# Kernel optimization log

Hardware: AMD Instinct MI355X
Metric: run time of the kernel (lower is better)

## Reference

```python
import jax, jax.numpy as jnp
import numpy as np

NH, NP, HD = 8, 4, 32  # num_heads, num_points, head_dim (C=256)


def setup_inputs() -> dict:
    key = jax.random.key(0)
    k = jax.random.split(key, 8)
    B, Nq, H, W, C = 4, 8192, 128, 128, 256
    query = jax.random.normal(k[0], (B, Nq, C), jnp.float32)
    reference_points = jax.random.uniform(k[1], (B, Nq, 2), jnp.float32)
    value = jax.random.normal(k[2], (B, H * W, C), jnp.float32)
    s = 1.0 / np.sqrt(C).astype(np.float32)
    W_off = jax.random.normal(k[3], (C, NH * NP * 2), jnp.float32) * s
    b_off = jax.random.normal(k[4], (NH * NP * 2,), jnp.float32) * 0.5
    W_attn = jax.random.normal(k[5], (C, NH * NP), jnp.float32) * s
    b_attn = jnp.zeros((NH * NP,), jnp.float32)
    W_val = jax.random.normal(k[6], (C, C), jnp.float32) * s
    b_val = jnp.zeros((C,), jnp.float32)
    W_out = jax.random.normal(k[7], (C, C), jnp.float32) * s
    b_out = jnp.zeros((C,), jnp.float32)
    return dict(query=query, reference_points=reference_points, value=value,
                W_off=W_off, b_off=b_off, W_attn=W_attn, b_attn=b_attn,
                W_val=W_val, b_val=b_val, W_out=W_out, b_out=b_out, Hs=H, Ws=W)


def reference(query, reference_points, value, W_off, b_off, W_attn, b_attn,
              W_val, b_val, W_out, b_out, Hs, Ws):
    B, Nq, C = query.shape
    # sampling offsets and attention weights from queries
    off = (query @ W_off + b_off).reshape(B, Nq, NH, NP, 2)
    attn = jax.nn.softmax((query @ W_attn + b_attn).reshape(B, Nq, NH, NP), axis=-1)
    off = jnp.stack([off[..., 0] / Ws * 0.1, off[..., 1] / Hs * 0.1], axis=-1)
    loc = jnp.clip(reference_points[:, :, None, None, :] + off, 0.0, 1.0)  # [B,Nq,NH,NP,2] (x,y)
    # project value and arrange per head: [B, NH, H*W, HD]
    v = (value @ W_val + b_val).reshape(B, Hs, Ws, NH, HD)
    v = v.transpose(0, 3, 1, 2, 4).reshape(B, NH, Hs * Ws, HD)
    # grid_sample bilinear, align_corners=False, padding_mode='border':
    # pixel coord = loc*size - 0.5, clamped to [0, size-1]
    gx = jnp.clip(loc[..., 0] * Ws - 0.5, 0.0, Ws - 1.0)
    gy = jnp.clip(loc[..., 1] * Hs - 0.5, 0.0, Hs - 1.0)
    x0 = jnp.floor(gx); y0 = jnp.floor(gy)
    fx = gx - x0; fy = gy - y0
    x0i = x0.astype(jnp.int32); y0i = y0.astype(jnp.int32)
    x1i = jnp.minimum(x0i + 1, Ws - 1); y1i = jnp.minimum(y0i + 1, Hs - 1)

    def flat(xi, yi):  # [B,Nq,NH,NP] -> [B,NH,Nq*NP]
        return (yi * Ws + xi).transpose(0, 2, 1, 3).reshape(B, NH, Nq * NP)

    def gather(idx):  # -> [B,NH,Nq*NP,HD]
        return jnp.take_along_axis(v, idx[..., None], axis=2)

    def wts(w):  # [B,Nq,NH,NP] -> [B,NH,Nq*NP,1]
        return w.transpose(0, 2, 1, 3).reshape(B, NH, Nq * NP, 1)

    samp = (wts((1 - fx) * (1 - fy)) * gather(flat(x0i, y0i))
            + wts(fx * (1 - fy)) * gather(flat(x1i, y0i))
            + wts((1 - fx) * fy) * gather(flat(x0i, y1i))
            + wts(fx * fy) * gather(flat(x1i, y1i)))
    samp = samp.reshape(B, NH, Nq, NP, HD)
    aw = attn.transpose(0, 2, 1, 3)[..., None]  # [B,NH,Nq,NP,1]
    out = (samp * aw).sum(axis=3)               # [B,NH,Nq,HD]
    out = out.transpose(0, 2, 1, 3).reshape(B, Nq, C)
    return out @ W_out + b_out
```

## Files before the change

### kernel.cpp

```cpp
#include <hip/hip_runtime.h>
#include <cstddef>

#define B_   4
#define NQ_  8192
#define C_   256
#define H_   128
#define W_   128
#define HW_  (H_ * W_)
#define NH_  8
#define NP_  4
#define HD_  32

typedef __attribute__((ext_vector_type(8))) short s16x8;
typedef __attribute__((ext_vector_type(4))) float f32x4;

__device__ __forceinline__ short f2bf(float x) {
    unsigned u = __float_as_uint(x);
    unsigned r = (u + 0x7FFFu + ((u >> 16) & 1u)) >> 16;
    return (short)r;
}
__device__ __forceinline__ void gload_lds16(const void* g, void* l) {
    __builtin_amdgcn_global_load_lds(
        (const __attribute__((address_space(1))) void*)g,
        (__attribute__((address_space(3))) void*)l, 16, 0, 0);
}

__global__ void prep_kernel(const float* __restrict__ Wv, const float* __restrict__ Wo,
                            const float* __restrict__ Woff, const float* __restrict__ Wattn,
                            const float* __restrict__ boff, const float* __restrict__ battn,
                            short* __restrict__ BtVal, short* __restrict__ BtOut,
                            short* __restrict__ BtOA, float* __restrict__ biasOA)
{
    const int b = blockIdx.x, t = threadIdx.x;
    if (b < 256) {
        const int n = b;
        BtVal[(size_t)n * 256 + t] = f2bf(Wv[(size_t)t * 256 + n]);
    } else if (b < 512) {
        const int n = b - 256;
        BtOut[(size_t)n * 256 + t] = f2bf(Wo[(size_t)t * 256 + n]);
    } else {
        const int n = b - 512;
        float v = (n < 64) ? Woff[(size_t)t * 64 + n]
                           : (n < 96 ? Wattn[(size_t)t * 32 + (n - 64)] : 0.f);
        BtOA[(size_t)n * 256 + t] = f2bf(v);
        if (t == 0) biasOA[n] = (n < 64) ? boff[n] : (n < 96 ? battn[n - 64] : 0.f);
    }
}

template<int AMODE, int OMODE>
__global__ __launch_bounds__(256)
void gemm_mfma(const void* __restrict__ Ap, const short* __restrict__ Bt,
               const float* __restrict__ bias, void* __restrict__ Cp, int ldc)
{
    __shared__ short As[128 * 32];
    __shared__ short Bs[128 * 32];
    const int tid = threadIdx.x;
    const int l = tid & 63;
    const int w = tid >> 6;
    const int wm = w >> 1, wn = w & 1;
    const int m0 = blockIdx.x * 128;
    const int n0 = blockIdx.y * 128;

    f32x4 acc[4][4];
#pragma unroll
    for (int i = 0; i < 4; ++i)
#pragma unroll
        for (int j = 0; j < 4; ++j) acc[i][j] = (f32x4)0.f;

    const int frag_r = l & 15;
    const int kslot  = (l >> 4) * 8;

    for (int k0 = 0; k0 < 256; k0 += 32) {
        __syncthreads();
#pragma unroll
        for (int r = 0; r < 2; ++r) {
            const int i = r * 256 + tid;
            const int row = i >> 2, cb = (i & 3) * 8;
            gload_lds16(&Bt[(size_t)(n0 + row) * 256 + k0 + cb],
                        (char*)Bs + r * 4096 + w * 1024);
        }
        if (AMODE == 0) {
            const short* A16 = (const short*)Ap;
#pragma unroll
            for (int r = 0; r < 2; ++r) {
                const int i = r * 256 + tid;
                const int row = i >> 2, cb = (i & 3) * 8;
                gload_lds16(&A16[(size_t)(m0 + row) * 256 + k0 + cb],
                            (char*)As + r * 4096 + w * 1024);
            }
        } else {
            const float* Af = (const float*)Ap;
            const int row = tid >> 1, half = tid & 1;
            const float* src = &Af[(size_t)(m0 + row) * 256 + k0 + half * 16];
            float4 f0 = ((const float4*)src)[0];
            float4 f1 = ((const float4*)src)[1];
            float4 f2 = ((const float4*)src)[2];
            float4 f3 = ((const float4*)src)[3];
            union { short s[8]; s16x8 v; } p0, p1;
            p0.s[0]=f2bf(f0.x); p0.s[1]=f2bf(f0.y); p0.s[2]=f2bf(f0.z); p0.s[3]=f2bf(f0.w);
            p0.s[4]=f2bf(f1.x); p0.s[5]=f2bf(f1.y); p0.s[6]=f2bf(f1.z); p0.s[7]=f2bf(f1.w);
            p1.s[0]=f2bf(f2.x); p1.s[1]=f2bf(f2.y); p1.s[2]=f2bf(f2.z); p1.s[3]=f2bf(f2.w);
            p1.s[4]=f2bf(f3.x); p1.s[5]=f2bf(f3.y); p1.s[6]=f2bf(f3.z); p1.s[7]=f2bf(f3.w);
            *(s16x8*)&As[row * 32 + half * 16]     = p0.v;
            *(s16x8*)&As[row * 32 + half * 16 + 8] = p1.v;
        }
        __syncthreads();
        s16x8 a[4], b[4];
#pragma unroll
        for (int mf = 0; mf < 4; ++mf)
            a[mf] = *(const s16x8*)&As[(wm * 64 + mf * 16 + frag_r) * 32 + kslot];
#pragma unroll
        for (int nf = 0; nf < 4; ++nf)
            b[nf] = *(const s16x8*)&Bs[(wn * 64 + nf * 16 + frag_r) * 32 + kslot];
#pragma unroll
        for (int mf = 0; mf < 4; ++mf)
#pragma unroll
            for (int nf = 0; nf < 4; ++nf)
                acc[mf][nf] = __builtin_amdgcn_mfma_f32_16x16x32_bf16(
                    a[mf], b[nf], acc[mf][nf], 0, 0, 0);
    }

    const int col_local = wn * 64 + (l & 15);
    const int rbase = wm * 64 + (l >> 4) * 4;
#pragma unroll
    for (int nf = 0; nf < 4; ++nf) {
        const int n = n0 + col_local + nf * 16;
        const float bs = bias[n];
#pragma unroll
        for (int mf = 0; mf < 4; ++mf) {
            const f32x4 v = acc[mf][nf];
#pragma unroll
            for (int rr = 0; rr < 4; ++rr) {
                const int m = m0 + rbase + mf * 16 + rr;
                const float o = v[rr] + bs;
                if (OMODE == 0) {
                    ((float*)Cp)[(size_t)m * ldc + n] = o;
                } else {
                    const int bb = m >> 14, pix = m & (HW_ - 1);
                    const int h = n >> 5, d = n & 31;
                    ((short*)Cp)[((size_t)(bb * NH_ + h) * HW_ + pix) * HD_ + d] = f2bf(o);
                }
            }
        }
    }
}

__global__ __launch_bounds__(256)
void sample_kernel(const float* __restrict__ oa,
                   const float* __restrict__ ref,
                   const short* __restrict__ vproj,
                   short* __restrict__ samp)
{
    __shared__ int4   s_idx[2][32];
    __shared__ float4 s_w[2][32];
    const int tid = threadIdx.x;
    const int q0 = blockIdx.x * 2;

    if (tid < 64) {
        const int qq = tid >> 5;
        const int hp = tid & 31;
        const int h = hp >> 2, p = hp & 3;
        const int q = q0 + qq;
        const float logit = oa[(size_t)q * 128 + 64 + h * 4 + p];
        float mx = fmaxf(logit, __shfl_xor(logit, 1));
        mx = fmaxf(mx, __shfl_xor(mx, 2));
        float e = __expf(logit - mx);
        float s = e + __shfl_xor(e, 1);
        s += __shfl_xor(s, 2);
        const float aw = e / s;

        const float ox = oa[(size_t)q * 128 + h * 8 + p * 2 + 0] * (0.1f / (float)W_);
        const float oy = oa[(size_t)q * 128 + h * 8 + p * 2 + 1] * (0.1f / (float)H_);
        const float lx = fminf(fmaxf(ref[(size_t)q * 2 + 0] + ox, 0.f), 1.f);
        const float ly = fminf(fmaxf(ref[(size_t)q * 2 + 1] + oy, 0.f), 1.f);
        const float gx = fminf(fmaxf(lx * (float)W_ - 0.5f, 0.f), (float)(W_ - 1));
        const float gy = fminf(fmaxf(ly * (float)H_ - 0.5f, 0.f), (float)(H_ - 1));
        const float x0f = floorf(gx), y0f = floorf(gy);
        const float fx = gx - x0f, fy = gy - y0f;
        const int x0 = (int)x0f, y0 = (int)y0f;
        const int x1 = min(x0 + 1, W_ - 1), y1 = min(y0 + 1, H_ - 1);
        s_idx[qq][hp] = make_int4((y0 * W_ + x0) * HD_, (y0 * W_ + x1) * HD_,
                                  (y1 * W_ + x0) * HD_, (y1 * W_ + x1) * HD_);
        const float gx1 = 1.f - fx, gy1 = 1.f - fy;
        s_w[qq][hp] = make_float4(aw * gx1 * gy1, aw * fx * gy1,
                                  aw * gx1 * fy,  aw * fx * fy);
    }
    __syncthreads();

    const int qq = tid >> 7;
    const int t = tid & 127;
    const int h = t >> 4;
    const int d0 = (t & 15) * 2;
    const int q = q0 + qq;
    const int b = q >> 13;
    const short* vh = vproj + (size_t)(b * NH_ + h) * (HW_ * HD_) + d0;

    float a0 = 0.f, a1 = 0.f;
#pragma unroll
    for (int p = 0; p < 4; ++p) {
        const int4   ii = s_idx[qq][h * 4 + p];
        const float4 ww = s_w[qq][h * 4 + p];
        unsigned v;
        v = *(const unsigned*)&vh[ii.x];
        a0 = fmaf(ww.x, __uint_as_float(v << 16), a0);
        a1 = fmaf(ww.x, __uint_as_float(v & 0xFFFF0000u), a1);
        v = *(const unsigned*)&vh[ii.y];
        a0 = fmaf(ww.y, __uint_as_float(v << 16), a0);
        a1 = fmaf(ww.y, __uint_as_float(v & 0xFFFF0000u), a1);
        v = *(const unsigned*)&vh[ii.z];
        a0 = fmaf(ww.z, __uint_as_float(v << 16), a0);
        a1 = fmaf(ww.z, __uint_as_float(v & 0xFFFF0000u), a1);
        v = *(const unsigned*)&vh[ii.w];
        a0 = fmaf(ww.w, __uint_as_float(v << 16), a0);
        a1 = fmaf(ww.w, __uint_as_float(v & 0xFFFF0000u), a1);
    }
    const unsigned lo = (unsigned)(unsigned short)f2bf(a0);
    const unsigned hi = (unsigned)(unsigned short)f2bf(a1);
    ((unsigned*)samp)[((size_t)q * 256 + h * HD_ + d0) >> 1] = lo | (hi << 16);
}

extern "C" void kernel_launch(void* const* d_in, const int* in_sizes, int n_in,
                              void* d_out, int out_size, void* d_ws, size_t ws_size,
                              hipStream_t stream)
{
    const float* query  = (const float*)d_in[0];
    const float* refpt  = (const float*)d_in[1];
    const float* value  = (const float*)d_in[2];
    const float* W_off  = (const float*)d_in[3];
    const float* b_off  = (const float*)d_in[4];
    const float* W_attn = (const float*)d_in[5];
    const float* b_attn = (const float*)d_in[6];
    const float* W_val  = (const float*)d_in[7];
    const float* b_val  = (const float*)d_in[8];
    const float* W_out  = (const float*)d_in[9];
    const float* b_out  = (const float*)d_in[10];
    float* out = (float*)d_out;

    char* ws = (char*)d_ws;
    short* vproj  = (short*)ws;
    short* samp   = (short*)(ws + (size_t)32 * 1024 * 1024);
    float* oa     = (float*)(ws + (size_t)48 * 1024 * 1024);
    short* BtVal  = (short*)(ws + (size_t)64 * 1024 * 1024);
    short* BtOut  = BtVal + 256 * 256;
    short* BtOA   = BtOut + 256 * 256;
    float* biasOA = (float*)(BtOA + 128 * 256);

    prep_kernel<<<640, 256, 0, stream>>>(W_val, W_out, W_off, W_attn,
                                         b_off, b_attn, BtVal, BtOut, BtOA, biasOA);

    gemm_mfma<1, 2><<<dim3((B_ * HW_) / 128, 2), 256, 0, stream>>>(
        value, BtVal, b_val, vproj, 0);

    gemm_mfma<1, 0><<<dim3((B_ * NQ_) / 128, 1), 256, 0, stream>>>(
        query, BtOA, biasOA, oa, 128);

    sample_kernel<<<(B_ * NQ_) / 2, 256, 0, stream>>>(oa, refpt, vproj, samp);

    gemm_mfma<0, 0><<<dim3((B_ * NQ_) / 128, 2), 256, 0, stream>>>(
        samp, BtOut, b_out, out, 256);
}
```

Baseline: 87.95 us.

## Double-buffer GEMM K-loop and merge value and query projections into one launch

The GEMM body now uses double-buffered LDS tiles. The next K-slice's global loads (async LDS loads for B, register loads for fp32 A) are issued before the current slice's MFMAs, which leaves one barrier per iteration instead of two. The value-projection and offset/attention GEMMs are fused into one 1280-block launch dispatched by block index, and launch bounds now request 4 blocks per CU. This is meant to hide global-load latency and cut one launch plus its tail, at the cost of doubled shared memory and more register pressure from holding the prefetched A values.

```diff
diff --git a/kernel.cpp b/kernel.cpp
--- a/kernel.cpp
+++ b/kernel.cpp
@@ -47,19 +47,16 @@
     }
 }
 
-template<int AMODE, int OMODE>
-__global__ __launch_bounds__(256)
-void gemm_mfma(const void* __restrict__ Ap, const short* __restrict__ Bt,
-               const float* __restrict__ bias, void* __restrict__ Cp, int ldc)
-{
-    __shared__ short As[128 * 32];
-    __shared__ short Bs[128 * 32];
+template<int AMODE>
+__device__ __forceinline__ void gemm_body(
+    const void* __restrict__ Ap, const short* __restrict__ Bt,
+    const float* __restrict__ bias, void* __restrict__ Cp,
+    int ldc, int omode, int m0, int n0, short* As, short* Bs)
+{
     const int tid = threadIdx.x;
     const int l = tid & 63;
     const int w = tid >> 6;
     const int wm = w >> 1, wn = w & 1;
-    const int m0 = blockIdx.x * 128;
-    const int n0 = blockIdx.y * 128;
 
     f32x4 acc[4][4];
 #pragma unroll
@@ -69,80 +66,142 @@
 
     const int frag_r = l & 15;
     const int kslot  = (l >> 4) * 8;
-
-    for (int k0 = 0; k0 < 256; k0 += 32) {
-        __syncthreads();
-#pragma unroll
-        for (int r = 0; r < 2; ++r) {
-            const int i = r * 256 + tid;
-            const int row = i >> 2, cb = (i & 3) * 8;
-            gload_lds16(&Bt[(size_t)(n0 + row) * 256 + k0 + cb],
-                        (char*)Bs + r * 4096 + w * 1024);
+    const int arow = tid >> 1, ahalf = tid & 1;
+    const float* Af = (const float*)Ap;
+    const short* A16 = (const short*)Ap;
+
+    float4 fA0, fA1, fA2, fA3;
+
+#define STAGE_B(k0, buf)                                                      \
+    _Pragma("unroll")                                                         \
+    for (int r = 0; r < 2; ++r) {                                             \
+        const int i = r * 256 + tid;                                          \
+        gload_lds16(&Bt[(size_t)(n0 + (i >> 2)) * 256 + (k0) + (i & 3) * 8],  \
+                    (char*)Bs + (buf) * 8192 + r * 4096 + w * 1024);          \
+    }
+#define STAGE_A_LDS(k0, buf)                                                  \
+    _Pragma("unroll")                                                         \
+    for (int r = 0; r < 2; ++r) {                                             \
+        const int i = r * 256 + tid;                                          \
+        gload_lds16(&A16[(size_t)(m0 + (i >> 2)) * 256 + (k0) + (i & 3) * 8], \
+                    (char*)As + (buf) * 8192 + r * 4096 + w * 1024);          \
+    }
+#define LOAD_A_REGS(k0)                                                       \
+    {                                                                         \
+        const float* src = &Af[(size_t)(m0 + arow) * 256 + (k0) + ahalf * 16];\
+        fA0 = ((const float4*)src)[0];                                        \
+        fA1 = ((const float4*)src)[1];                                        \
+        fA2 = ((const float4*)src)[2];                                        \
+        fA3 = ((const float4*)src)[3];                                        \
+    }
+#define WRITE_A(buf)                                                          \
+    {                                                                         \
+        union { short s[8]; s16x8 v; } p0, p1;                                \
+        p0.s[0]=f2bf(fA0.x); p0.s[1]=f2bf(fA0.y); p0.s[2]=f2bf(fA0.z); p0.s[3]=f2bf(fA0.w); \
+        p0.s[4]=f2bf(fA1.x); p0.s[5]=f2bf(fA1.y); p0.s[6]=f2bf(fA1.z); p0.s[7]=f2bf(fA1.w); \
+        p1.s[0]=f2bf(fA2.x); p1.s[1]=f2bf(fA2.y); p1.s[2]=f2bf(fA2.z); p1.s[3]=f2bf(fA2.w); \
+        p1.s[4]=f2bf(fA3.x); p1.s[5]=f2bf(fA3.y); p1.s[6]=f2bf(fA3.z); p1.s[7]=f2bf(fA3.w); \
+        *(s16x8*)&As[(buf) * 4096 + arow * 32 + ahalf * 16]     = p0.v;       \
+        *(s16x8*)&As[(buf) * 4096 + arow * 32 + ahalf * 16 + 8] = p1.v;       \
+    }
+
+    STAGE_B(0, 0);
+    if (AMODE == 0) { STAGE_A_LDS(0, 0); }
+    else            { LOAD_A_REGS(0); WRITE_A(0); }
+    __syncthreads();
+
+#pragma unroll
+    for (int k = 0; k < 8; ++k) {
+        const int cur = k & 1, nxt = cur ^ 1;
+        if (k < 7) {
+            STAGE_B((k + 1) * 32, nxt);
+            if (AMODE == 0) { STAGE_A_LDS((k + 1) * 32, nxt); }
+            else            { LOAD_A_REGS((k + 1) * 32); }
         }
-        if (AMODE == 0) {
-            const short* A16 = (const short*)Ap;
-#pragma unroll
-            for (int r = 0; r < 2; ++r) {
-                const int i = r * 256 + tid;
-                const int row = i >> 2, cb = (i & 3) * 8;
-                gload_lds16(&A16[(size_t)(m0 + row) * 256 + k0 + cb],
-                            (char*)As + r * 4096 + w * 1024);
-            }
-        } else {
-            const float* Af = (const float*)Ap;
-            const int row = tid >> 1, half = tid & 1;
-            const float* src = &Af[(size_t)(m0 + row) * 256 + k0 + half * 16];
-            float4 f0 = ((const float4*)src)[0];
-            float4 f1 = ((const float4*)src)[1];
-            float4 f2 = ((const float4*)src)[2];
-            float4 f3 = ((const float4*)src)[3];
-            union { short s[8]; s16x8 v; } p0, p1;
-            p0.s[0]=f2bf(f0.x); p0.s[1]=f2bf(f0.y); p0.s[2]=f2bf(f0.z); p0.s[3]=f2bf(f0.w);
-            p0.s[4]=f2bf(f1.x); p0.s[5]=f2bf(f1.y); p0.s[6]=f2bf(f1.z); p0.s[7]=f2bf(f1.w);
-            p1.s[0]=f2bf(f2.x); p1.s[1]=f2bf(f2.y); p1.s[2]=f2bf(f2.z); p1.s[3]=f2bf(f2.w);
-            p1.s[4]=f2bf(f3.x); p1.s[5]=f2bf(f3.y); p1.s[6]=f2bf(f3.z); p1.s[7]=f2bf(f3.w);
-            *(s16x8*)&As[row * 32 + half * 16]     = p0.v;
-            *(s16x8*)&As[row * 32 + half * 16 + 8] = p1.v;
-        }
-        __syncthreads();
         s16x8 a[4], b[4];
 #pragma unroll
         for (int mf = 0; mf < 4; ++mf)
-            a[mf] = *(const s16x8*)&As[(wm * 64 + mf * 16 + frag_r) * 32 + kslot];
+            a[mf] = *(const s16x8*)&As[cur * 4096 + (wm * 64 + mf * 16 + frag_r) * 32 + kslot];
 #pragma unroll
         for (int nf = 0; nf < 4; ++nf)
-            b[nf] = *(const s16x8*)&Bs[(wn * 64 + nf * 16 + frag_r) * 32 + kslot];
+            b[nf] = *(const s16x8*)&Bs[cur * 4096 + (wn * 64 + nf * 16 + frag_r) * 32 + kslot];
 #pragma unroll
         for (int mf = 0; mf < 4; ++mf)
 #pragma unroll
             for (int nf = 0; nf < 4; ++nf)
                 acc[mf][nf] = __builtin_amdgcn_mfma_f32_16x16x32_bf16(
                     a[mf], b[nf], acc[mf][nf], 0, 0, 0);
-    }
+        if (k < 7) {
+            if (AMODE == 1) WRITE_A(nxt);
+            __syncthreads();
+        }
+    }
+#undef STAGE_B
+#undef STAGE_A_LDS
+#undef LOAD_A_REGS
+#undef WRITE_A
 
     const int col_local = wn * 64 + (l & 15);
     const int rbase = wm * 64 + (l >> 4) * 4;
-#pragma unroll
-    for (int nf = 0; nf < 4; ++nf) {
-        const int n = n0 + col_local + nf * 16;
-        const float bs = bias[n];
-#pragma unroll
-        for (int mf = 0; mf < 4; ++mf) {
-            const f32x4 v = acc[mf][nf];
-#pragma unroll
-            for (int rr = 0; rr < 4; ++rr) {
-                const int m = m0 + rbase + mf * 16 + rr;
-                const float o = v[rr] + bs;
-                if (OMODE == 0) {
-                    ((float*)Cp)[(size_t)m * ldc + n] = o;
-                } else {
+    if (omode == 0) {
+#pragma unroll
+        for (int nf = 0; nf < 4; ++nf) {
+            const int n = n0 + col_local + nf * 16;
+            const float bs = bias[n];
+#pragma unroll
+            for (int mf = 0; mf < 4; ++mf) {
+                const f32x4 v = acc[mf][nf];
+#pragma unroll
+                for (int rr = 0; rr < 4; ++rr)
+                    ((float*)Cp)[(size_t)(m0 + rbase + mf * 16 + rr) * ldc + n] = v[rr] + bs;
+            }
+        }
+    } else {
+#pragma unroll
+        for (int nf = 0; nf < 4; ++nf) {
+            const int n = n0 + col_local + nf * 16;
+            const float bs = bias[n];
+            const int h = n >> 5, d = n & 31;
+#pragma unroll
+            for (int mf = 0; mf < 4; ++mf) {
+                const f32x4 v = acc[mf][nf];
+#pragma unroll
+                for (int rr = 0; rr < 4; ++rr) {
+                    const int m = m0 + rbase + mf * 16 + rr;
                     const int bb = m >> 14, pix = m & (HW_ - 1);
-                    const int h = n >> 5, d = n & 31;
-                    ((short*)Cp)[((size_t)(bb * NH_ + h) * HW_ + pix) * HD_ + d] = f2bf(o);
+                    ((short*)Cp)[((size_t)(bb * NH_ + h) * HW_ + pix) * HD_ + d] = f2bf(v[rr] + bs);
                 }
             }
         }
     }
+}
+
+__global__ __launch_bounds__(256, 4)
+void gemm_k1k2a(const float* __restrict__ value, const short* __restrict__ BtVal,
+                const float* __restrict__ b_val, short* __restrict__ vproj,
+                const float* __restrict__ query, const short* __restrict__ BtOA,
+                const float* __restrict__ biasOA, float* __restrict__ oa)
+{
+    __shared__ short As[2 * 4096];
+    __shared__ short Bs[2 * 4096];
+    const int bid = blockIdx.x;
+    if (bid < 1024) {
+        gemm_body<1>(value, BtVal, b_val, vproj, 0, 2,
+                     (bid >> 1) * 128, (bid & 1) * 128, As, Bs);
+    } else {
+        gemm_body<1>(query, BtOA, biasOA, oa, 128, 0,
+                     (bid - 1024) * 128, 0, As, Bs);
+    }
+}
+
+__global__ __launch_bounds__(256, 4)
+void gemm_k3(const short* __restrict__ samp, const short* __restrict__ BtOut,
+             const float* __restrict__ b_out, float* __restrict__ out)
+{
+    __shared__ short As[2 * 4096];
+    __shared__ short Bs[2 * 4096];
+    gemm_body<0>(samp, BtOut, b_out, out, 256, 0,
+                 (blockIdx.x >> 1) * 128, (blockIdx.x & 1) * 128, As, Bs);
 }
 
 __global__ __launch_bounds__(256)
@@ -248,14 +307,10 @@
     prep_kernel<<<640, 256, 0, stream>>>(W_val, W_out, W_off, W_attn,
                                          b_off, b_attn, BtVal, BtOut, BtOA, biasOA);
 
-    gemm_mfma<1, 2><<<dim3((B_ * HW_) / 128, 2), 256, 0, stream>>>(
-        value, BtVal, b_val, vproj, 0);
-
-    gemm_mfma<1, 0><<<dim3((B_ * NQ_) / 128, 1), 256, 0, stream>>>(
-        query, BtOA, biasOA, oa, 128);
+    gemm_k1k2a<<<1280, 256, 0, stream>>>(value, BtVal, b_val, vproj,
+                                         query, BtOA, biasOA, oa);
 
     sample_kernel<<<(B_ * NQ_) / 2, 256, 0, stream>>>(oa, refpt, vproj, samp);
 
-    gemm_mfma<0, 0><<<dim3((B_ * NQ_) / 128, 2), 256, 0, stream>>>(
-        samp, BtOut, b_out, out, 256);
-}
+    gemm_k3<<<512, 256, 0, stream>>>(samp, BtOut, b_out, out);
+}
```

Result: faster. 84.64 us (-3.8%).

## Replace tiled GEMM with B-stationary LDS kernel loading A straight into registers

Applied to the files above, without the earlier changes.

Replaces the K-looped 128x128 tiled MFMA GEMM with a kernel that loads the whole 128x256 bf16 weight panel into swizzled LDS once per block. Each wave then streams 16-row A strips directly from global memory into registers and runs all K steps without per-step barriers. Blocks are remapped across XCDs for the value projection, and the offset/attention GEMM now skips storing the unused padded columns. The aims are to remove repeated syncthreads and LDS staging of A and to reuse the weights across many rows. The cost is 64KB of LDS per block, which limits occupancy, and uncoalesced A loads that go straight to registers.

```diff
diff --git a/kernel.cpp b/kernel.cpp
--- a/kernel.cpp
+++ b/kernel.cpp
@@ -47,98 +47,94 @@
     }
 }
 
-template<int AMODE, int OMODE>
-__global__ __launch_bounds__(256)
-void gemm_mfma(const void* __restrict__ Ap, const short* __restrict__ Bt,
-               const float* __restrict__ bias, void* __restrict__ Cp, int ldc)
-{
-    __shared__ short As[128 * 32];
-    __shared__ short Bs[128 * 32];
+template<int ADT, int OM, int ROWS, int HALVES>
+__global__ __launch_bounds__(256, 2)
+void gemm_bstat(const void* __restrict__ Ap, const short* __restrict__ Bt0,
+                const float* __restrict__ bias, void* __restrict__ Cp,
+                int ldc, int nstore)
+{
+    __shared__ short Bs[128 * 256];
     const int tid = threadIdx.x;
     const int l = tid & 63;
     const int w = tid >> 6;
-    const int wm = w >> 1, wn = w & 1;
-    const int m0 = blockIdx.x * 128;
-    const int n0 = blockIdx.y * 128;
-
-    f32x4 acc[4][4];
-#pragma unroll
-    for (int i = 0; i < 4; ++i)
-#pragma unroll
-        for (int j = 0; j < 4; ++j) acc[i][j] = (f32x4)0.f;
-
-    const int frag_r = l & 15;
-    const int kslot  = (l >> 4) * 8;
-
-    for (int k0 = 0; k0 < 256; k0 += 32) {
-        __syncthreads();
-#pragma unroll
-        for (int r = 0; r < 2; ++r) {
-            const int i = r * 256 + tid;
-            const int row = i >> 2, cb = (i & 3) * 8;
-            gload_lds16(&Bt[(size_t)(n0 + row) * 256 + k0 + cb],
-                        (char*)Bs + r * 4096 + w * 1024);
+
+    int mch, half;
+    if (HALVES == 2) {
+        const int xcd = blockIdx.x & 7;
+        const int lix = blockIdx.x >> 3;
+        mch = xcd * 32 + (lix >> 1);
+        half = lix & 1;
+    } else {
+        mch = blockIdx.x;
+        half = 0;
+    }
+    const int m0 = mch * ROWS;
+    const int n0 = half * 128;
+    const char* BtB = (const char*)(Bt0 + (size_t)half * 128 * 256);
+
+    {
+        const int r7 = tid >> 5;
+        const int scol = ((tid & 31) * 16) ^ (r7 << 4);
+#pragma unroll
+        for (int i = 0; i < 16; ++i)
+            gload_lds16(BtB + (size_t)(i * 8 + r7) * 512 + scol,
+                        (char*)Bs + i * 4096 + w * 1024);
+    }
+    __syncthreads();
+
+    const int arow_l = l & 15;
+    const int kb     = (l >> 4) * 8;
+    const float* Af  = (const float*)Ap;
+    const short* A16 = (const short*)Ap;
+
+    float bias_r[8];
+#pragma unroll
+    for (int nf = 0; nf < 8; ++nf)
+        bias_r[nf] = bias[n0 + nf * 16 + arow_l];
+
+    for (int s = w; s < ROWS / 16; s += 4) {
+        const int mrow = m0 + s * 16 + arow_l;
+        s16x8 a[8];
+        if (ADT == 0) {
+#pragma unroll
+            for (int kk = 0; kk < 8; ++kk)
+                a[kk] = *(const s16x8*)(A16 + (size_t)mrow * 256 + kk * 32 + kb);
+        } else {
+#pragma unroll
+            for (int kk = 0; kk < 8; ++kk) {
+                const float* ap = Af + (size_t)mrow * 256 + kk * 32 + kb;
+                const float4 u0 = ((const float4*)ap)[0];
+                const float4 u1 = ((const float4*)ap)[1];
+                union { short s[8]; s16x8 v; } pk;
+                pk.s[0]=f2bf(u0.x); pk.s[1]=f2bf(u0.y); pk.s[2]=f2bf(u0.z); pk.s[3]=f2bf(u0.w);
+                pk.s[4]=f2bf(u1.x); pk.s[5]=f2bf(u1.y); pk.s[6]=f2bf(u1.z); pk.s[7]=f2bf(u1.w);
+                a[kk] = pk.v;
+            }
         }
-        if (AMODE == 0) {
-            const short* A16 = (const short*)Ap;
-#pragma unroll
-            for (int r = 0; r < 2; ++r) {
-                const int i = r * 256 + tid;
-                const int row = i >> 2, cb = (i & 3) * 8;
-                gload_lds16(&A16[(size_t)(m0 + row) * 256 + k0 + cb],
-                            (char*)As + r * 4096 + w * 1024);
+#pragma unroll
+        for (int nf = 0; nf < 8; ++nf) {
+            f32x4 acc = (f32x4)0.f;
+#pragma unroll
+            for (int kk = 0; kk < 8; ++kk) {
+                const int brow = nf * 16 + arow_l;
+                const int cswz = (kk * 64 + (l >> 4) * 16) ^ ((arow_l & 7) << 4);
+                const s16x8 b = *(const s16x8*)((const char*)Bs + brow * 512 + cswz);
+                acc = __builtin_amdgcn_mfma_f32_16x16x32_bf16(a[kk], b, acc, 0, 0, 0);
             }
-        } else {
-            const float* Af = (const float*)Ap;
-            const int row = tid >> 1, half = tid & 1;
-            const float* src = &Af[(size_t)(m0 + row) * 256 + k0 + half * 16];
-            float4 f0 = ((const float4*)src)[0];
-            float4 f1 = ((const float4*)src)[1];
-            float4 f2 = ((const float4*)src)[2];
-            float4 f3 = ((const float4*)src)[3];
-            union { short s[8]; s16x8 v; } p0, p1;
-            p0.s[0]=f2bf(f0.x); p0.s[1]=f2bf(f0.y); p0.s[2]=f2bf(f0.z); p0.s[3]=f2bf(f0.w);
-            p0.s[4]=f2bf(f1.x); p0.s[5]=f2bf(f1.y); p0.s[6]=f2bf(f1.z); p0.s[7]=f2bf(f1.w);
-            p1.s[0]=f2bf(f2.x); p1.s[1]=f2bf(f2.y); p1.s[2]=f2bf(f2.z); p1.s[3]=f2bf(f2.w);
-            p1.s[4]=f2bf(f3.x); p1.s[5]=f2bf(f3.y); p1.s[6]=f2bf(f3.z); p1.s[7]=f2bf(f3.w);
-            *(s16x8*)&As[row * 32 + half * 16]     = p0.v;
-            *(s16x8*)&As[row * 32 + half * 16 + 8] = p1.v;
-        }
-        __syncthreads();
-        s16x8 a[4], b[4];
-#pragma unroll
-        for (int mf = 0; mf < 4; ++mf)
-            a[mf] = *(const s16x8*)&As[(wm * 64 + mf * 16 + frag_r) * 32 + kslot];
-#pragma unroll
-        for (int nf = 0; nf < 4; ++nf)
-            b[nf] = *(const s16x8*)&Bs[(wn * 64 + nf * 16 + frag_r) * 32 + kslot];
-#pragma unroll
-        for (int mf = 0; mf < 4; ++mf)
-#pragma unroll
-            for (int nf = 0; nf < 4; ++nf)
-                acc[mf][nf] = __builtin_amdgcn_mfma_f32_16x16x32_bf16(
-                    a[mf], b[nf], acc[mf][nf], 0, 0, 0);
-    }
-
-    const int col_local = wn * 64 + (l & 15);
-    const int rbase = wm * 64 + (l >> 4) * 4;
-#pragma unroll
-    for (int nf = 0; nf < 4; ++nf) {
-        const int n = n0 + col_local + nf * 16;
-        const float bs = bias[n];
-#pragma unroll
-        for (int mf = 0; mf < 4; ++mf) {
-            const f32x4 v = acc[mf][nf];
-#pragma unroll
-            for (int rr = 0; rr < 4; ++rr) {
-                const int m = m0 + rbase + mf * 16 + rr;
-                const float o = v[rr] + bs;
-                if (OMODE == 0) {
-                    ((float*)Cp)[(size_t)m * ldc + n] = o;
-                } else {
-                    const int bb = m >> 14, pix = m & (HW_ - 1);
-                    const int h = n >> 5, d = n & 31;
-                    ((short*)Cp)[((size_t)(bb * NH_ + h) * HW_ + pix) * HD_ + d] = f2bf(o);
+            if (nf < nstore) {
+                const int n = n0 + nf * 16 + arow_l;
+                const float bs = bias_r[nf];
+#pragma unroll
+                for (int rr = 0; rr < 4; ++rr) {
+                    const int m = m0 + s * 16 + (l >> 4) * 4 + rr;
+                    const float o = acc[rr] + bs;
+                    if (OM == 0) {
+                        ((float*)Cp)[(size_t)m * ldc + n] = o;
+                    } else {
+                        const int bb = m >> 14, pix = m & (HW_ - 1);
+                        const int h = n >> 5, d = n & 31;
+                        ((short*)Cp)[((size_t)(bb * NH_ + h) * HW_ + pix) * HD_ + d] = f2bf(o);
+                    }
                 }
             }
         }
@@ -248,14 +244,14 @@
     prep_kernel<<<640, 256, 0, stream>>>(W_val, W_out, W_off, W_attn,
                                          b_off, b_attn, BtVal, BtOut, BtOA, biasOA);
 
-    gemm_mfma<1, 2><<<dim3((B_ * HW_) / 128, 2), 256, 0, stream>>>(
-        value, BtVal, b_val, vproj, 0);
-
-    gemm_mfma<1, 0><<<dim3((B_ * NQ_) / 128, 1), 256, 0, stream>>>(
-        query, BtOA, biasOA, oa, 128);
+    gemm_bstat<1, 2, 256, 2><<<512, 256, 0, stream>>>(
+        value, BtVal, b_val, vproj, 0, 8);
+
+    gemm_bstat<1, 0, 64, 1><<<512, 256, 0, stream>>>(
+        query, BtOA, biasOA, oa, 128, 6);
 
     sample_kernel<<<(B_ * NQ_) / 2, 256, 0, stream>>>(oa, refpt, vproj, samp);
 
-    gemm_mfma<0, 0><<<dim3((B_ * NQ_) / 128, 2), 256, 0, stream>>>(
-        samp, BtOut, b_out, out, 256);
-}
+    gemm_bstat<0, 0, 128, 2><<<512, 256, 0, stream>>>(
+        samp, BtOut, b_out, out, 256, 8);
+}
```

New measurement: 135.6 us. 54.2% more time.
